# Kernel tuning notes

Measured on AMD Instinct MI355X. Metric: run time of the kernel, lower is better.

The kernel has to match this reference:

```python
import jax, jax.numpy as jnp
import numpy as np


def setup_inputs() -> dict:
    key = jax.random.key(0)
    ks = jax.random.split(key, 7)
    B, H, W = 32, 28, 28
    C3, C4 = 1024, 2048
    C = C3 + C4            # 3072
    L1 = 9                 # num_landmarks + 1
    A, NC = 312, 200
    return {
        "l3": jax.random.normal(ks[0], (B, C3, H, W), jnp.float32),
        "l4": jax.random.normal(ks[1], (B, C4, H // 2, W // 2), jnp.float32),
        "conv_w": jax.random.normal(ks[2], (L1, C), jnp.float32) * 0.02,
        "modulation": jnp.ones((1, C, L1), jnp.float32),
        "attr_w": jax.random.normal(ks[3], (A, C), jnp.float32) * 0.02,
        "attr_b": jnp.zeros((A,), jnp.float32),
        "class_w": jax.random.normal(ks[4], (NC, A), jnp.float32) * 0.02,
    }


def reference(l3, l4, conv_w, modulation, attr_w, attr_b, class_w):
    b, c3, h, w = l3.shape
    # F.interpolate(l4, (h, w), mode='bilinear', align_corners=False)
    l4_up = jax.image.resize(l4, (b, l4.shape[1], h, w), method="bilinear")
    x = jnp.concatenate([l4_up, l3], axis=1)            # (b, 3072, h, w)

    # 1x1 conv: ab[b,l,h,w] = sum_c w[l,c] * x[b,c,h,w]
    ab = jnp.einsum("lc,bchw->blhw", conv_w, x)
    b_sq = jnp.sum(x * x, axis=1, keepdims=True)        # (b,1,h,w)
    a_sq = jnp.sum(conv_w, axis=1)[None, :, None, None]  # (1,L+1,1,1)  (matches torch: weight.sum(1), NOT squared)
    maps = jax.nn.softmax(-(b_sq - 2.0 * ab + a_sq), axis=1)  # Softmax2d = softmax over channels

    # (maps[:,None] * x[:,:,None]).mean((-1,-2))  ->  batched GEMM over spatial dim
    all_features = jnp.einsum("blhw,bchw->bcl", maps, x) / (h * w)  # (b, c, L+1)

    mod = all_features * modulation                     # dropout is identity at eval
    # permute(0,2,1)[:, :-1, :].mean(1) == mean over landmark dim excluding background
    mean_features = jnp.mean(mod[:, :, :-1], axis=2)    # (b, c)

    attr_scores = mean_features @ attr_w.T + attr_b      # (b, 312)
    class_scores = attr_scores @ class_w.T               # (b, 200)
    return attr_scores, class_scores, maps, all_features
```

## Files before the change

### kernel.cpp

```cpp
#include <hip/hip_runtime.h>
#include <math.h>

#define B_    32
#define C3_   1024
#define C4_   2048
#define C_    3072
#define P_    784
#define Q_    196
#define L_    9
#define NG_   25088
#define A_    312
#define NC_   200

#define ATTR_OFF  0
#define CLASS_OFF 9984
#define MAPS_OFF  16384
#define AF_OFF    242176

#define ASQ_OFF   0
#define MF_OFF    16
#define PART3_OFF 98320
#define PAF_OFF   98320
#define Y4P_OFF   (PART3_OFF + 16 * 9 * NG_)
#define LOGITS_OFF Y4P_OFF
#define Y_OFF     (Y4P_OFF + 32 * 32 * 9 * Q_)
#define MP_OFF    (Y_OFF + 32 * 9 * Q_)

typedef __attribute__((ext_vector_type(8))) short bf16x8;
typedef __attribute__((ext_vector_type(4))) float f32x4;

__device__ __forceinline__ short f2bf(float f) {
    union { float f; unsigned u; } v; v.f = f;
    unsigned r = v.u + 0x7FFFu + ((v.u >> 16) & 1u);
    return (short)(r >> 16);
}

#define GLDS16(gp, lp) __builtin_amdgcn_global_load_lds(                    \
        (const __attribute__((address_space(1))) unsigned int*)(gp),        \
        (__attribute__((address_space(3))) unsigned int*)(lp), 16, 0, 0)

__global__ __launch_bounds__(256, 5) void kA(
        const float* __restrict__ l3, const float* __restrict__ l4,
        const float* __restrict__ conv_w,
        float* __restrict__ part3, float* __restrict__ y4p) {
    __shared__ float X[2][16 * 256];
    int bid = blockIdx.x;
    int t = threadIdx.x;
    int wave = t >> 6, lane = t & 63;

    bool isl3 = (bid < 1568);
    int slab = 0, g0 = 0, b = 0, grp = 0, cbase_w;
    const float* gbase;
    size_t rowpitch;
    if (isl3) {
        slab = bid / 98;
        g0 = (bid % 98) * 256;
        int gidx = g0 + lane * 4;
        int bb = gidx / 784, px = gidx % 784;
        gbase = l3 + ((size_t)bb * C3_ + slab * 64) * P_ + px;
        rowpitch = P_;
        cbase_w = C4_ + slab * 64;
    } else {
        int idx = bid - 1568;
        b = idx >> 5; grp = idx & 31;
        int q = lane * 4;
        if (q > 192) q = 192;
        gbase = l4 + ((size_t)b * C4_ + grp * 64) * Q_ + q;
        rowpitch = Q_;
        cbase_w = grp * 64;
    }

#pragma unroll
    for (int r = 0; r < 4; ++r) {
        int row = wave * 4 + r;
        GLDS16(gbase + (size_t)row * rowpitch, &X[0][row * 256]);
    }

    float acc[9];
#pragma unroll
    for (int l = 0; l < 9; ++l) acc[l] = 0.f;

#pragma unroll
    for (int j = 0; j < 4; ++j) {
        const int cur = j & 1;
        if (j < 3) {
#pragma unroll
            for (int r = 0; r < 4; ++r) {
                int row = wave * 4 + r;
                int ch = (j + 1) * 16 + row;
                GLDS16(gbase + (size_t)ch * rowpitch, &X[cur ^ 1][row * 256]);
            }
            asm volatile("s_waitcnt vmcnt(4)" ::: "memory");
        } else {
            asm volatile("s_waitcnt vmcnt(0)" ::: "memory");
        }
        __builtin_amdgcn_s_barrier();

        if (isl3 || t < 196) {
#pragma unroll
            for (int c = 0; c < 16; ++c) {
                float x = X[cur][c * 256 + t];
#pragma unroll
                for (int l = 0; l < 9; ++l)
                    acc[l] = fmaf(conv_w[(size_t)l * C_ + cbase_w + j * 16 + c],
                                  x, acc[l]);
            }
        }
        __builtin_amdgcn_s_barrier();
    }

    if (isl3) {
        float* op = part3 + (size_t)(slab * 9) * NG_ + g0 + t;
#pragma unroll
        for (int l = 0; l < 9; ++l) op[(size_t)l * NG_] = acc[l];
    } else if (t < 196) {
        float* op = y4p + ((size_t)(b * 32 + grp) * 9) * Q_ + t;
#pragma unroll
        for (int l = 0; l < 9; ++l) op[l * Q_] = acc[l];
    }
}

__global__ __launch_bounds__(256) void kB(const float* __restrict__ y4p,
                                          const float* __restrict__ conv_w,
                                          float* __restrict__ Y,
                                          float* __restrict__ asq) {
    if (blockIdx.x == 221) {
        __shared__ float red[256];
        int t = threadIdx.x;
        for (int l = 0; l < L_; ++l) {
            float s = 0.f;
            for (int c = t; c < C_; c += 256) s += conv_w[l * C_ + c];
            red[t] = s; __syncthreads();
            for (int o = 128; o > 0; o >>= 1) {
                if (t < o) red[t] += red[t + o];
                __syncthreads();
            }
            if (t == 0) asq[l] = red[0];
            __syncthreads();
        }
        return;
    }
    int tid = blockIdx.x * 256 + threadIdx.x;
    if (tid >= 32 * 9 * Q_) return;
    int b = tid / (9 * Q_);
    int r = tid % (9 * Q_);
    float s = 0.f;
#pragma unroll
    for (int grp = 0; grp < 32; ++grp)
        s += y4p[(size_t)(b * 32 + grp) * (9 * Q_) + r];
    Y[(size_t)b * (9 * Q_) + r] = s;
}

__global__ __launch_bounds__(256) void kC1(const float* __restrict__ part3,
                                           const float* __restrict__ Y,
                                           const float* __restrict__ asq,
                                           float* __restrict__ logits) {
    int idx = blockIdx.x * 256 + threadIdx.x;
    int l = idx / NG_, g = idx % NG_;
    int b = g / P_, p = g % P_;
    int yy = p / 28, xx = p % 28;
    float sy = 0.5f * yy - 0.25f, sx = 0.5f * xx - 0.25f;
    float fyf = floorf(sy), fxf = floorf(sx);
    float fy = sy - fyf, fx = sx - fxf;
    int ya = max(0, (int)fyf), yb = min(13, (int)fyf + 1);
    int xa = max(0, (int)fxf), xb = min(13, (int)fxf + 1);
    float w00 = (1.f - fy) * (1.f - fx), w01 = (1.f - fy) * fx;
    float w10 = fy * (1.f - fx),         w11 = fy * fx;
    const float* Yl = Y + ((size_t)b * 9 + l) * Q_;
    float ab4 = w00 * Yl[ya * 14 + xa] + w01 * Yl[ya * 14 + xb]
              + w10 * Yl[yb * 14 + xa] + w11 * Yl[yb * 14 + xb];
    float ab3 = 0.f;
#pragma unroll
    for (int sl = 0; sl < 16; ++sl)
        ab3 += part3[(size_t)(sl * 9 + l) * NG_ + g];
    logits[idx] = 2.f * (ab4 + ab3) - asq[l];
}

__global__ __launch_bounds__(256) void kC2(const float* __restrict__ logits,
                                           float* __restrict__ out_maps) {
    int g = blockIdx.x * 256 + threadIdx.x;
    int b = g / P_, p = g % P_;
    float v[9];
#pragma unroll
    for (int l = 0; l < 9; ++l) v[l] = logits[(size_t)l * NG_ + g];
    float m = v[0];
#pragma unroll
    for (int l = 1; l < 9; ++l) m = fmaxf(m, v[l]);
    float sum = 0.f;
#pragma unroll
    for (int l = 0; l < 9; ++l) { v[l] = expf(v[l] - m); sum += v[l]; }
    float inv = 1.f / sum;
#pragma unroll
    for (int l = 0; l < 9; ++l)
        out_maps[(size_t)b * (L_ * P_) + l * P_ + p] = v[l] * inv;
}

__device__ __forceinline__ int adj_taps(int q, int* ys, float* wy) {
    if (q == 0)  { ys[0] = 0;  wy[0] = 1.00f; ys[1] = 1;  wy[1] = 0.75f;
                   ys[2] = 2;  wy[2] = 0.25f; return 3; }
    if (q == 13) { ys[0] = 25; wy[0] = 0.25f; ys[1] = 26; wy[1] = 0.75f;
                   ys[2] = 27; wy[2] = 1.00f; return 3; }
    ys[0] = 2 * q - 1; wy[0] = 0.25f;
    ys[1] = 2 * q;     wy[1] = 0.75f;
    ys[2] = 2 * q + 1; wy[2] = 0.75f;
    ys[3] = 2 * q + 2; wy[3] = 0.25f;
    return 4;
}

__global__ __launch_bounds__(256) void kD(const float* __restrict__ maps,
                                          float* __restrict__ Mp) {
    int tid = blockIdx.x * 256 + threadIdx.x;
    if (tid >= 32 * 9 * Q_) return;
    int b = tid / (9 * Q_);
    int r = tid % (9 * Q_);
    int l = r / Q_, q = r % Q_;
    int qy = q / 14, qx = q % 14;
    int ys[4], xs[4]; float wy[4], wx[4];
    int ny = adj_taps(qy, ys, wy);
    int nx = adj_taps(qx, xs, wx);
    const float* mrow = maps + (size_t)b * (L_ * P_) + l * P_;
    float s = 0.f;
    for (int i = 0; i < ny; ++i) {
        float rs = 0.f;
        for (int j = 0; j < nx; ++j)
            rs = fmaf(wx[j], mrow[ys[i] * 28 + xs[j]], rs);
        s = fmaf(wy[i], rs, s);
    }
    Mp[(size_t)b * (9 * Q_) + r] = s;
}

#define SA 232
__global__ __launch_bounds__(256) void kE(
        const float* __restrict__ l3, const float* __restrict__ l4,
        const float* __restrict__ maps, const float* __restrict__ Mp,
        float* __restrict__ out_af, float* __restrict__ paf) {
    __shared__ short As[64 * SA];
    __shared__ short Bs[16 * SA];
    int bid = blockIdx.x;
    int t = threadIdx.x;
    int wave = t >> 6, lane = t & 63;
    int row16 = lane & 15, quad = lane >> 4;

    const float* xsrc; size_t xstride;
    const float* bsrc; size_t bstride;
    int b, c0, h;
    bool isl4 = (bid < 1024);
    if (isl4) {
        b = bid >> 5;
        c0 = (bid & 31) * 64;
        h = 0;
        xsrc = l4 + ((size_t)b * C4_ + c0) * Q_;
        xstride = Q_;
        bsrc = Mp + (size_t)b * (9 * Q_);
        bstride = Q_;
    } else {
        int idx = bid - 1024;
        b = idx >> 6;
        c0 = ((idx >> 2) & 15) * 64;
        h = idx & 3;
        xsrc = l3 + ((size_t)b * C3_ + c0) * P_ + h * Q_;
        xstride = P_;
        bsrc = maps + (size_t)b * (L_ * P_) + h * Q_;
        bstride = P_;
    }

    for (int i = t; i < 64 * 49; i += 256) {
        int r = i / 49, j = (i % 49) * 4;
        float4 v = *(const float4*)(xsrc + (size_t)r * xstride + j);
        ushort4 o;
        o.x = (unsigned short)f2bf(v.x); o.y = (unsigned short)f2bf(v.y);
        o.z = (unsigned short)f2bf(v.z); o.w = (unsigned short)f2bf(v.w);
        *(ushort4*)(As + r * SA + j) = o;
    }
    for (int i = t; i < 64 * 9; i += 256) {
        int r = i / 9, j = 196 + (i % 9) * 4;
        *(ushort4*)(As + r * SA + j) = make_ushort4(0, 0, 0, 0);
    }
    for (int i = t; i < 16 * 58; i += 256) {
        int r = i / 58, j = (i % 58) * 4;
        ushort4 o = make_ushort4(0, 0, 0, 0);
        if (r < 9 && j < 196) {
            float4 v = *(const float4*)(bsrc + (size_t)r * bstride + j);
            o.x = (unsigned short)f2bf(v.x); o.y = (unsigned short)f2bf(v.y);
            o.z = (unsigned short)f2bf(v.z); o.w = (unsigned short)f2bf(v.w);
        }
        *(ushort4*)(Bs + r * SA + j) = o;
    }
    __syncthreads();

    const short* arow = As + (wave * 16 + row16) * SA;
    const short* brow = Bs + row16 * SA;
    f32x4 acc = {0.f, 0.f, 0.f, 0.f};
#pragma unroll
    for (int k0 = 0; k0 < 224; k0 += 32) {
        bf16x8 a = *(const bf16x8*)(arow + k0 + quad * 8);
        bf16x8 bv = *(const bf16x8*)(brow + k0 + quad * 8);
        acc = __builtin_amdgcn_mfma_f32_16x16x32_bf16(a, bv, acc, 0, 0, 0);
    }
    int l = row16;
    if (l < 9) {
        int c = c0 + wave * 16 + quad * 4;
        if (isl4) {
            size_t base = ((size_t)b * C_ + c) * 9 + l;
#pragma unroll
            for (int r = 0; r < 4; ++r)
                out_af[base + (size_t)r * 9] = acc[r] * (1.f / 784.f);
        } else {
            size_t base = ((size_t)(h * B_ + b) * C3_ + c) * 9 + l;
#pragma unroll
            for (int r = 0; r < 4; ++r)
                paf[base + (size_t)r * 9] = acc[r];
        }
    }
}

__global__ __launch_bounds__(256) void kMF(const float* __restrict__ paf,
                                           const float* __restrict__ mod,
                                           float* __restrict__ out_af,
                                           float* __restrict__ mf) {
    int i = blockIdx.x * 256 + threadIdx.x;
    if (i >= B_ * C_) return;
    int b = i / C_, c = i % C_;
    float af[9];
    if (c < C4_) {
#pragma unroll
        for (int l = 0; l < 9; ++l) af[l] = out_af[(size_t)i * 9 + l];
    } else {
        int c3 = c - C4_;
#pragma unroll
        for (int l = 0; l < 9; ++l) {
            float s = 0.f;
#pragma unroll
            for (int hh = 0; hh < 4; ++hh)
                s += paf[((size_t)(hh * B_ + b) * C3_ + c3) * 9 + l];
            af[l] = s * (1.f / 784.f);
            out_af[(size_t)i * 9 + l] = af[l];
        }
    }
    const float* m = mod + (size_t)c * 9;
    float s = 0.f;
#pragma unroll
    for (int l = 0; l < 8; ++l) s = fmaf(af[l], m[l], s);
    mf[i] = s * 0.125f;
}

__global__ __launch_bounds__(256) void kF(
        const float* __restrict__ mf, const float* __restrict__ attr_w,
        const float* __restrict__ attr_b, float* __restrict__ out_attr) {
    int idx = blockIdx.x * 4 + (threadIdx.x >> 6);
    int lane = threadIdx.x & 63;
    int b = idx / A_, a = idx % A_;
    const float4* wr = (const float4*)(attr_w + (size_t)a * C_);
    const float4* mr = (const float4*)(mf + (size_t)b * C_);
    float acc = 0.f;
    for (int j = lane; j < C_ / 4; j += 64) {
        float4 w = wr[j], m = mr[j];
        acc += w.x * m.x + w.y * m.y + w.z * m.z + w.w * m.w;
    }
    acc += __shfl_xor(acc, 1);  acc += __shfl_xor(acc, 2);
    acc += __shfl_xor(acc, 4);  acc += __shfl_xor(acc, 8);
    acc += __shfl_xor(acc, 16); acc += __shfl_xor(acc, 32);
    if (lane == 0) out_attr[idx] = acc + attr_b[a];
}

__global__ __launch_bounds__(256) void kG(
        const float* __restrict__ attr, const float* __restrict__ class_w,
        float* __restrict__ out_class) {
    int idx = blockIdx.x * 4 + (threadIdx.x >> 6);
    int lane = threadIdx.x & 63;
    int b = idx / NC_, n = idx % NC_;
    float acc = 0.f;
    for (int a = lane; a < A_; a += 64)
        acc += attr[b * A_ + a] * class_w[n * A_ + a];
    acc += __shfl_xor(acc, 1);  acc += __shfl_xor(acc, 2);
    acc += __shfl_xor(acc, 4);  acc += __shfl_xor(acc, 8);
    acc += __shfl_xor(acc, 16); acc += __shfl_xor(acc, 32);
    if (lane == 0) out_class[idx] = acc;
}

extern "C" void kernel_launch(void* const* d_in, const int* in_sizes, int n_in,
                              void* d_out, int out_size, void* d_ws, size_t ws_size,
                              hipStream_t stream) {
    (void)in_sizes; (void)n_in; (void)out_size; (void)ws_size;
    const float* l3         = (const float*)d_in[0];
    const float* l4         = (const float*)d_in[1];
    const float* conv_w     = (const float*)d_in[2];
    const float* modulation = (const float*)d_in[3];
    const float* attr_w     = (const float*)d_in[4];
    const float* attr_b     = (const float*)d_in[5];
    const float* class_w    = (const float*)d_in[6];
    float* out = (float*)d_out;
    float* ws  = (float*)d_ws;
    float* asq    = ws + ASQ_OFF;
    float* mf     = ws + MF_OFF;
    float* part3  = ws + PART3_OFF;
    float* paf    = ws + PAF_OFF;
    float* y4p    = ws + Y4P_OFF;
    float* logits = ws + LOGITS_OFF;
    float* Y      = ws + Y_OFF;
    float* Mp     = ws + MP_OFF;

    kA<<<2592, 256, 0, stream>>>(l3, l4, conv_w, part3, y4p);
    kB<<<222, 256, 0, stream>>>(y4p, conv_w, Y, asq);
    kC1<<<882, 256, 0, stream>>>(part3, Y, asq, logits);
    kC2<<<98, 256, 0, stream>>>(logits, out + MAPS_OFF);
    kD<<<221, 256, 0, stream>>>(out + MAPS_OFF, Mp);
    kE<<<3072, 256, 0, stream>>>(l3, l4, out + MAPS_OFF, Mp, out + AF_OFF, paf);
    kMF<<<384, 256, 0, stream>>>(paf, modulation, out + AF_OFF, mf);
    kF<<<(B_ * A_) / 4, 256, 0, stream>>>(mf, attr_w, attr_b, out + ATTR_OFF);
    kG<<<(B_ * NC_) / 4, 256, 0, stream>>>(out + ATTR_OFF, class_w,
                                           out + CLASS_OFF);
}
```

Baseline: 306.8 us.

## Replace partial-sum buffers with atomics and fuse reductions into fewer kernels

kA now accumulates its conv partial sums straight into the logits and Y buffers with atomicAdd, after a new zero-init kernel clears them and computes asq. That removes the kB reduction kernel and the large part3/y4p workspace traffic, and kC1 and kC2 merge into one kC that does the bilinear add and the softmax. kE now loops over the four l3 spatial chunks itself with double-buffered LDS staging, and it computes the modulated mean features in-kernel through shuffle reductions, which removes the paf buffer and the kMF kernel. The trade-off is atomic contention (16 l3 channel slabs per logits element, 32 channel groups per Y element) and a small extra launch. Float atomics also make the summation order nondeterministic.

```diff
diff --git a/kernel.cpp b/kernel.cpp
--- a/kernel.cpp
+++ b/kernel.cpp
@@ -19,11 +19,8 @@
 
 #define ASQ_OFF   0
 #define MF_OFF    16
-#define PART3_OFF 98320
-#define PAF_OFF   98320
-#define Y4P_OFF   (PART3_OFF + 16 * 9 * NG_)
-#define LOGITS_OFF Y4P_OFF
-#define Y_OFF     (Y4P_OFF + 32 * 32 * 9 * Q_)
+#define LOGITS_OFF 98320
+#define Y_OFF     (LOGITS_OFF + 9 * NG_)
 #define MP_OFF    (Y_OFF + 32 * 9 * Q_)
 
 typedef __attribute__((ext_vector_type(8))) short bf16x8;
@@ -39,10 +36,35 @@
         (const __attribute__((address_space(1))) unsigned int*)(gp),        \
         (__attribute__((address_space(3))) unsigned int*)(lp), 16, 0, 0)
 
+__global__ __launch_bounds__(256) void zK(const float* __restrict__ conv_w,
+                                          float* __restrict__ Y,
+                                          float* __restrict__ logits,
+                                          float* __restrict__ asq) {
+    if (blockIdx.x == 0) {
+        __shared__ float red[256];
+        int t = threadIdx.x;
+        for (int l = 0; l < L_; ++l) {
+            float s = 0.f;
+            for (int c = t; c < C_; c += 256) s += conv_w[l * C_ + c];
+            red[t] = s; __syncthreads();
+            for (int o = 128; o > 0; o >>= 1) {
+                if (t < o) red[t] += red[t + o];
+                __syncthreads();
+            }
+            if (t == 0) asq[l] = red[0];
+            __syncthreads();
+        }
+        return;
+    }
+    int i = (blockIdx.x - 1) * 256 + threadIdx.x;
+    if (i < 32 * 9 * Q_) Y[i] = 0.f;
+    else if (i < 32 * 9 * Q_ + 9 * NG_) logits[i - 32 * 9 * Q_] = 0.f;
+}
+
 __global__ __launch_bounds__(256, 5) void kA(
         const float* __restrict__ l3, const float* __restrict__ l4,
         const float* __restrict__ conv_w,
-        float* __restrict__ part3, float* __restrict__ y4p) {
+        float* __restrict__ logits, float* __restrict__ Y) {
     __shared__ float X[2][16 * 256];
     int bid = blockIdx.x;
     int t = threadIdx.x;
@@ -110,53 +132,21 @@
     }
 
     if (isl3) {
-        float* op = part3 + (size_t)(slab * 9) * NG_ + g0 + t;
-#pragma unroll
-        for (int l = 0; l < 9; ++l) op[(size_t)l * NG_] = acc[l];
+#pragma unroll
+        for (int l = 0; l < 9; ++l)
+            atomicAdd(&logits[(size_t)l * NG_ + g0 + t], 2.f * acc[l]);
     } else if (t < 196) {
-        float* op = y4p + ((size_t)(b * 32 + grp) * 9) * Q_ + t;
-#pragma unroll
-        for (int l = 0; l < 9; ++l) op[l * Q_] = acc[l];
-    }
-}
-
-__global__ __launch_bounds__(256) void kB(const float* __restrict__ y4p,
-                                          const float* __restrict__ conv_w,
-                                          float* __restrict__ Y,
-                                          float* __restrict__ asq) {
-    if (blockIdx.x == 221) {
-        __shared__ float red[256];
-        int t = threadIdx.x;
-        for (int l = 0; l < L_; ++l) {
-            float s = 0.f;
-            for (int c = t; c < C_; c += 256) s += conv_w[l * C_ + c];
-            red[t] = s; __syncthreads();
-            for (int o = 128; o > 0; o >>= 1) {
-                if (t < o) red[t] += red[t + o];
-                __syncthreads();
-            }
-            if (t == 0) asq[l] = red[0];
-            __syncthreads();
-        }
-        return;
-    }
-    int tid = blockIdx.x * 256 + threadIdx.x;
-    if (tid >= 32 * 9 * Q_) return;
-    int b = tid / (9 * Q_);
-    int r = tid % (9 * Q_);
-    float s = 0.f;
-#pragma unroll
-    for (int grp = 0; grp < 32; ++grp)
-        s += y4p[(size_t)(b * 32 + grp) * (9 * Q_) + r];
-    Y[(size_t)b * (9 * Q_) + r] = s;
-}
-
-__global__ __launch_bounds__(256) void kC1(const float* __restrict__ part3,
-                                           const float* __restrict__ Y,
-                                           const float* __restrict__ asq,
-                                           float* __restrict__ logits) {
-    int idx = blockIdx.x * 256 + threadIdx.x;
-    int l = idx / NG_, g = idx % NG_;
+#pragma unroll
+        for (int l = 0; l < 9; ++l)
+            atomicAdd(&Y[((size_t)b * 9 + l) * Q_ + t], acc[l]);
+    }
+}
+
+__global__ __launch_bounds__(256) void kC(const float* __restrict__ logits,
+                                          const float* __restrict__ Y,
+                                          const float* __restrict__ asq,
+                                          float* __restrict__ out_maps) {
+    int g = blockIdx.x * 256 + threadIdx.x;
     int b = g / P_, p = g % P_;
     int yy = p / 28, xx = p % 28;
     float sy = 0.5f * yy - 0.25f, sx = 0.5f * xx - 0.25f;
@@ -166,23 +156,14 @@
     int xa = max(0, (int)fxf), xb = min(13, (int)fxf + 1);
     float w00 = (1.f - fy) * (1.f - fx), w01 = (1.f - fy) * fx;
     float w10 = fy * (1.f - fx),         w11 = fy * fx;
-    const float* Yl = Y + ((size_t)b * 9 + l) * Q_;
-    float ab4 = w00 * Yl[ya * 14 + xa] + w01 * Yl[ya * 14 + xb]
-              + w10 * Yl[yb * 14 + xa] + w11 * Yl[yb * 14 + xb];
-    float ab3 = 0.f;
-#pragma unroll
-    for (int sl = 0; sl < 16; ++sl)
-        ab3 += part3[(size_t)(sl * 9 + l) * NG_ + g];
-    logits[idx] = 2.f * (ab4 + ab3) - asq[l];
-}
-
-__global__ __launch_bounds__(256) void kC2(const float* __restrict__ logits,
-                                           float* __restrict__ out_maps) {
-    int g = blockIdx.x * 256 + threadIdx.x;
-    int b = g / P_, p = g % P_;
     float v[9];
 #pragma unroll
-    for (int l = 0; l < 9; ++l) v[l] = logits[(size_t)l * NG_ + g];
+    for (int l = 0; l < 9; ++l) {
+        const float* Yl = Y + ((size_t)b * 9 + l) * Q_;
+        float ab4 = w00 * Yl[ya * 14 + xa] + w01 * Yl[ya * 14 + xb]
+                  + w10 * Yl[yb * 14 + xa] + w11 * Yl[yb * 14 + xb];
+        v[l] = logits[(size_t)l * NG_ + g] + 2.f * ab4 - asq[l];
+    }
     float m = v[0];
 #pragma unroll
     for (int l = 1; l < 9; ++l) m = fmaxf(m, v[l]);
@@ -230,118 +211,139 @@
 }
 
 #define SA 232
-__global__ __launch_bounds__(256) void kE(
+__global__ __launch_bounds__(256, 2) void kE(
         const float* __restrict__ l3, const float* __restrict__ l4,
         const float* __restrict__ maps, const float* __restrict__ Mp,
-        float* __restrict__ out_af, float* __restrict__ paf) {
-    __shared__ short As[64 * SA];
-    __shared__ short Bs[16 * SA];
+        const float* __restrict__ mod,
+        float* __restrict__ out_af, float* __restrict__ mf) {
+    __shared__ short As[2][64 * SA];
+    __shared__ short Bs[2][16 * SA];
     int bid = blockIdx.x;
     int t = threadIdx.x;
     int wave = t >> 6, lane = t & 63;
     int row16 = lane & 15, quad = lane >> 4;
 
-    const float* xsrc; size_t xstride;
-    const float* bsrc; size_t bstride;
-    int b, c0, h;
-    bool isl4 = (bid < 1024);
-    if (isl4) {
-        b = bid >> 5;
-        c0 = (bid & 31) * 64;
-        h = 0;
+    bool isl3 = (bid < 512);
+    int b, c0, nchunk, cglob0, pitch;
+    const float* xsrc; const float* bsrc;
+    if (isl3) {
+        b = bid >> 4; c0 = (bid & 15) * 64; nchunk = 4;
+        xsrc = l3 + ((size_t)b * C3_ + c0) * P_;
+        bsrc = maps + (size_t)b * (L_ * P_);
+        pitch = P_;
+        cglob0 = C4_ + c0;
+    } else {
+        int idx = bid - 512;
+        b = idx >> 5; c0 = (idx & 31) * 64; nchunk = 1;
         xsrc = l4 + ((size_t)b * C4_ + c0) * Q_;
-        xstride = Q_;
         bsrc = Mp + (size_t)b * (9 * Q_);
-        bstride = Q_;
-    } else {
-        int idx = bid - 1024;
-        b = idx >> 6;
-        c0 = ((idx >> 2) & 15) * 64;
-        h = idx & 3;
-        xsrc = l3 + ((size_t)b * C3_ + c0) * P_ + h * Q_;
-        xstride = P_;
-        bsrc = maps + (size_t)b * (L_ * P_) + h * Q_;
-        bstride = P_;
-    }
-
-    for (int i = t; i < 64 * 49; i += 256) {
-        int r = i / 49, j = (i % 49) * 4;
-        float4 v = *(const float4*)(xsrc + (size_t)r * xstride + j);
-        ushort4 o;
-        o.x = (unsigned short)f2bf(v.x); o.y = (unsigned short)f2bf(v.y);
-        o.z = (unsigned short)f2bf(v.z); o.w = (unsigned short)f2bf(v.w);
-        *(ushort4*)(As + r * SA + j) = o;
-    }
-    for (int i = t; i < 64 * 9; i += 256) {
-        int r = i / 9, j = 196 + (i % 9) * 4;
-        *(ushort4*)(As + r * SA + j) = make_ushort4(0, 0, 0, 0);
-    }
-    for (int i = t; i < 16 * 58; i += 256) {
-        int r = i / 58, j = (i % 58) * 4;
-        ushort4 o = make_ushort4(0, 0, 0, 0);
-        if (r < 9 && j < 196) {
-            float4 v = *(const float4*)(bsrc + (size_t)r * bstride + j);
-            o.x = (unsigned short)f2bf(v.x); o.y = (unsigned short)f2bf(v.y);
-            o.z = (unsigned short)f2bf(v.z); o.w = (unsigned short)f2bf(v.w);
-        }
-        *(ushort4*)(Bs + r * SA + j) = o;
-    }
+        pitch = Q_;
+        cglob0 = c0;
+    }
+
+#pragma unroll
+    for (int it = 0; it < 5; ++it) {
+        int i = t + it * 256;
+        if (i < 1152) {
+            int br = i / 9;
+            int j = 196 + (i % 9) * 4;
+            *(ushort4*)(&As[br >> 6][(br & 63) * SA + j]) =
+                make_ushort4(0, 0, 0, 0);
+        }
+    }
+
+    auto stage = [&](int cc, int buf) {
+        int koff = cc * 196;
+        float4 va[13];
+#pragma unroll
+        for (int it = 0; it < 13; ++it) {
+            int i = t + it * 256;
+            if (i < 3136) {
+                int r = i / 49, j = (i % 49) * 4;
+                va[it] = *(const float4*)(xsrc + (size_t)r * pitch + koff + j);
+            }
+        }
+        float4 vb[4];
+#pragma unroll
+        for (int it = 0; it < 4; ++it) {
+            int i = t + it * 256;
+            if (i < 928) {
+                int r = i / 58, j = (i % 58) * 4;
+                if (r < 9 && j < 196)
+                    vb[it] = *(const float4*)(bsrc + (size_t)r * pitch + koff + j);
+                else
+                    vb[it] = make_float4(0.f, 0.f, 0.f, 0.f);
+            }
+        }
+#pragma unroll
+        for (int it = 0; it < 13; ++it) {
+            int i = t + it * 256;
+            if (i < 3136) {
+                int r = i / 49, j = (i % 49) * 4;
+                ushort4 o;
+                o.x = (unsigned short)f2bf(va[it].x);
+                o.y = (unsigned short)f2bf(va[it].y);
+                o.z = (unsigned short)f2bf(va[it].z);
+                o.w = (unsigned short)f2bf(va[it].w);
+                *(ushort4*)(&As[buf][r * SA + j]) = o;
+            }
+        }
+#pragma unroll
+        for (int it = 0; it < 4; ++it) {
+            int i = t + it * 256;
+            if (i < 928) {
+                int r = i / 58, j = (i % 58) * 4;
+                ushort4 o;
+                o.x = (unsigned short)f2bf(vb[it].x);
+                o.y = (unsigned short)f2bf(vb[it].y);
+                o.z = (unsigned short)f2bf(vb[it].z);
+                o.w = (unsigned short)f2bf(vb[it].w);
+                *(ushort4*)(&Bs[buf][r * SA + j]) = o;
+            }
+        }
+    };
+
+    stage(0, 0);
     __syncthreads();
 
-    const short* arow = As + (wave * 16 + row16) * SA;
-    const short* brow = Bs + row16 * SA;
     f32x4 acc = {0.f, 0.f, 0.f, 0.f};
-#pragma unroll
-    for (int k0 = 0; k0 < 224; k0 += 32) {
-        bf16x8 a = *(const bf16x8*)(arow + k0 + quad * 8);
-        bf16x8 bv = *(const bf16x8*)(brow + k0 + quad * 8);
-        acc = __builtin_amdgcn_mfma_f32_16x16x32_bf16(a, bv, acc, 0, 0, 0);
-    }
+    for (int cc = 0; cc < nchunk; ++cc) {
+        int cur = cc & 1;
+        if (cc + 1 < nchunk) stage(cc + 1, cur ^ 1);
+        const short* arow = &As[cur][(wave * 16 + row16) * SA];
+        const short* brow = &Bs[cur][row16 * SA];
+#pragma unroll
+        for (int k0 = 0; k0 < 224; k0 += 32) {
+            bf16x8 a = *(const bf16x8*)(arow + k0 + quad * 8);
+            bf16x8 bv = *(const bf16x8*)(brow + k0 + quad * 8);
+            acc = __builtin_amdgcn_mfma_f32_16x16x32_bf16(a, bv, acc, 0, 0, 0);
+        }
+        __syncthreads();
+    }
+
     int l = row16;
+    int cg = cglob0 + wave * 16 + quad * 4;
+    float afv[4];
+#pragma unroll
+    for (int r = 0; r < 4; ++r) afv[r] = acc[r] * (1.f / 784.f);
     if (l < 9) {
-        int c = c0 + wave * 16 + quad * 4;
-        if (isl4) {
-            size_t base = ((size_t)b * C_ + c) * 9 + l;
-#pragma unroll
-            for (int r = 0; r < 4; ++r)
-                out_af[base + (size_t)r * 9] = acc[r] * (1.f / 784.f);
-        } else {
-            size_t base = ((size_t)(h * B_ + b) * C3_ + c) * 9 + l;
-#pragma unroll
-            for (int r = 0; r < 4; ++r)
-                paf[base + (size_t)r * 9] = acc[r];
-        }
-    }
-}
-
-__global__ __launch_bounds__(256) void kMF(const float* __restrict__ paf,
-                                           const float* __restrict__ mod,
-                                           float* __restrict__ out_af,
-                                           float* __restrict__ mf) {
-    int i = blockIdx.x * 256 + threadIdx.x;
-    if (i >= B_ * C_) return;
-    int b = i / C_, c = i % C_;
-    float af[9];
-    if (c < C4_) {
-#pragma unroll
-        for (int l = 0; l < 9; ++l) af[l] = out_af[(size_t)i * 9 + l];
-    } else {
-        int c3 = c - C4_;
-#pragma unroll
-        for (int l = 0; l < 9; ++l) {
-            float s = 0.f;
-#pragma unroll
-            for (int hh = 0; hh < 4; ++hh)
-                s += paf[((size_t)(hh * B_ + b) * C3_ + c3) * 9 + l];
-            af[l] = s * (1.f / 784.f);
-            out_af[(size_t)i * 9 + l] = af[l];
-        }
-    }
-    const float* m = mod + (size_t)c * 9;
-    float s = 0.f;
-#pragma unroll
-    for (int l = 0; l < 8; ++l) s = fmaf(af[l], m[l], s);
-    mf[i] = s * 0.125f;
+        size_t base = ((size_t)b * C_ + cg) * 9 + l;
+#pragma unroll
+        for (int r = 0; r < 4; ++r) out_af[base + (size_t)r * 9] = afv[r];
+    }
+    float term[4];
+#pragma unroll
+    for (int r = 0; r < 4; ++r)
+        term[r] = (l < 8) ? afv[r] * mod[(size_t)(cg + r) * 9 + l] : 0.f;
+#pragma unroll
+    for (int s = 1; s < 16; s <<= 1)
+#pragma unroll
+        for (int r = 0; r < 4; ++r) term[r] += __shfl_xor(term[r], s);
+    if (row16 == 0) {
+#pragma unroll
+        for (int r = 0; r < 4; ++r)
+            mf[(size_t)b * C_ + cg + r] = term[r] * 0.125f;
+    }
 }
 
 __global__ __launch_bounds__(256) void kF(
@@ -393,20 +395,16 @@
     float* ws  = (float*)d_ws;
     float* asq    = ws + ASQ_OFF;
     float* mf     = ws + MF_OFF;
-    float* part3  = ws + PART3_OFF;
-    float* paf    = ws + PAF_OFF;
-    float* y4p    = ws + Y4P_OFF;
     float* logits = ws + LOGITS_OFF;
     float* Y      = ws + Y_OFF;
     float* Mp     = ws + MP_OFF;
 
-    kA<<<2592, 256, 0, stream>>>(l3, l4, conv_w, part3, y4p);
-    kB<<<222, 256, 0, stream>>>(y4p, conv_w, Y, asq);
-    kC1<<<882, 256, 0, stream>>>(part3, Y, asq, logits);
-    kC2<<<98, 256, 0, stream>>>(logits, out + MAPS_OFF);
+    zK<<<1104, 256, 0, stream>>>(conv_w, Y, logits, asq);
+    kA<<<2592, 256, 0, stream>>>(l3, l4, conv_w, logits, Y);
+    kC<<<98, 256, 0, stream>>>(logits, Y, asq, out + MAPS_OFF);
     kD<<<221, 256, 0, stream>>>(out + MAPS_OFF, Mp);
-    kE<<<3072, 256, 0, stream>>>(l3, l4, out + MAPS_OFF, Mp, out + AF_OFF, paf);
-    kMF<<<384, 256, 0, stream>>>(paf, modulation, out + AF_OFF, mf);
+    kE<<<1536, 256, 0, stream>>>(l3, l4, out + MAPS_OFF, Mp, modulation,
+                                 out + AF_OFF, mf);
     kF<<<(B_ * A_) / 4, 256, 0, stream>>>(mf, attr_w, attr_b, out + ATTR_OFF);
     kG<<<(B_ * NC_) / 4, 256, 0, stream>>>(out + ATTR_OFF, class_w,
                                            out + CLASS_OFF);
```

Measured after the change: 312.5 us. No clear change (+1.8%).
